# Performance work log

Measured on AMD Instinct MI355X. Metric: run time of the kernel, lower is better.

Reference implementation:

```python
import jax, jax.numpy as jnp
import numpy as np

OUT_FEATURES = 4096
IN_FEATURES = 4096
GROUP_SIZE = 128
NUM_GROUPS = IN_FEATURES // GROUP_SIZE  # 32
PACKED_SIZE = OUT_FEATURES * IN_FEATURES // 8  # 2097152


def setup_inputs() -> dict:
    key = jax.random.key(0)
    k1, k2, k3, k4 = jax.random.split(key, 4)
    x = jax.random.normal(k1, (2, 512, IN_FEATURES), dtype=jnp.float32)
    # random packed 4-bit weights (8 nibbles per int32)
    w_packed = jax.random.randint(k2, (PACKED_SIZE,), jnp.iinfo(jnp.int32).min,
                                  jnp.iinfo(jnp.int32).max, dtype=jnp.int32)
    w_scale = jax.random.uniform(k3, (OUT_FEATURES, NUM_GROUPS), dtype=jnp.float32) * 0.05
    w_zero = jax.random.randint(k4, (OUT_FEATURES, NUM_GROUPS), 0, 8, dtype=jnp.int32)
    return {"x": x, "w_packed": w_packed, "w_scale": w_scale, "w_zero": w_zero}


def _unpack_dequant(w_packed, w_scale, w_zero):
    # Extract 8 nibbles per int32: (v >> (i*4)) & 0xF, i = 0..7
    shifts = jnp.arange(8, dtype=jnp.int32) * 4
    nibbles = (w_packed[:, None] >> shifts[None, :]) & 15  # [packed, 8]
    w4 = nibbles.reshape(-1)  # [out*in], values 0..15
    w4 = jnp.where(w4 >= 8, w4 - 16, w4)  # signed 4-bit -> [-8, 7]
    w_int = w4.reshape(OUT_FEATURES, NUM_GROUPS, GROUP_SIZE).astype(jnp.float32)
    # per-(row, group) dequant: (q - zero) * scale
    w = (w_int - w_zero[:, :, None].astype(jnp.float32)) * w_scale[:, :, None]
    return w.reshape(OUT_FEATURES, IN_FEATURES)


def reference(x, w_packed, w_scale, w_zero):
    weight = _unpack_dequant(w_packed, w_scale, w_zero).astype(x.dtype)
    # F.linear: y = x @ W^T
    return jnp.einsum('bsi,oi->bso', x, weight)
```

## Files before the change

### kernel.cpp

```cpp
#include <hip/hip_runtime.h>
#include <stdint.h>

#define IN_F 4096
#define OUT_F 4096
#define NG 32

typedef __attribute__((ext_vector_type(8))) _Float16 half8;
typedef __attribute__((ext_vector_type(2))) _Float16 half2t;
typedef __attribute__((ext_vector_type(4))) float floatx4;

__global__ __launch_bounds__(256) void prep_kernel(
    const float* __restrict__ x, _Float16* __restrict__ Xh,
    const float* __restrict__ wscale, const int* __restrict__ wzero,
    uint2* __restrict__ SZ, int nxb) {
  int b = blockIdx.x;
  if (b < nxb) {
    int i = b * 256 + threadIdx.x;
    const float4* x4 = (const float4*)x;
    float4 a = x4[2 * i];
    float4 c = x4[2 * i + 1];
    uint4 o;
    o.x = __builtin_bit_cast(unsigned, __builtin_amdgcn_cvt_pkrtz(a.x, c.x));
    o.y = __builtin_bit_cast(unsigned, __builtin_amdgcn_cvt_pkrtz(a.y, c.y));
    o.z = __builtin_bit_cast(unsigned, __builtin_amdgcn_cvt_pkrtz(a.z, c.z));
    o.w = __builtin_bit_cast(unsigned, __builtin_amdgcn_cvt_pkrtz(a.w, c.w));
    ((uint4*)Xh)[i] = o;
  } else {
    int i = (b - nxb) * 256 + threadIdx.x;
    float s = wscale[i];
    int zp = wzero[i];
    _Float16 sh = (_Float16)s;
    _Float16 ch = (_Float16)(float)(1032 + zp);
    unsigned s2 = (unsigned)__builtin_bit_cast(unsigned short, sh) * 0x10001u;
    unsigned c2 = (unsigned)__builtin_bit_cast(unsigned short, ch) * 0x10001u;
    SZ[i] = make_uint2(s2, c2);
  }
}

#define NSTEP 32

__device__ __forceinline__ uint4 dequant8(unsigned v, uint2 szv) {
  unsigned tx = v ^ 0x88888888u;
  half2t s2 = __builtin_bit_cast(half2t, szv.x);
  half2t c2 = __builtin_bit_cast(half2t, szv.y);
  unsigned p0 = (tx & 0x000F000Fu) | 0x64006400u;
  unsigned p1 = ((tx >> 4) & 0x000F000Fu) | 0x64006400u;
  unsigned p2 = ((tx >> 8) & 0x000F000Fu) | 0x64006400u;
  unsigned p3 = ((tx >> 12) & 0x000F000Fu) | 0x64006400u;
  half2t w0 = (__builtin_bit_cast(half2t, p0) - c2) * s2;
  half2t w1 = (__builtin_bit_cast(half2t, p1) - c2) * s2;
  half2t w2 = (__builtin_bit_cast(half2t, p2) - c2) * s2;
  half2t w3 = (__builtin_bit_cast(half2t, p3) - c2) * s2;
  uint4 o;
  o.x = __builtin_bit_cast(unsigned, w0);
  o.y = __builtin_bit_cast(unsigned, w1);
  o.z = __builtin_bit_cast(unsigned, w2);
  o.w = __builtin_bit_cast(unsigned, w3);
  return o;
}

__global__ __launch_bounds__(512, 2) void gemm_fused(
    const _Float16* __restrict__ A, const int* __restrict__ wp,
    const uint2* __restrict__ SZ, float* __restrict__ out,
    int M, int N, int K) {
  __shared__ __align__(16) _Float16 Alds[4 * 8192];
  __shared__ __align__(16) _Float16 Blds[4 * 8192];

  int t = threadIdx.x;
  int wave = t >> 6, lane = t & 63;
  int h = wave >> 2, w2 = wave & 3;
  int wm = (w2 >> 1) * 64, wn = (w2 & 1) * 64;
  int r = lane & 15, quad = lane >> 4, rb = r & 7;
  int bm = blockIdx.y * 128, bn = blockIdx.x * 128;

  floatx4 acc[4][4] = {};

  int kc = t & 7;
  int row0 = t >> 3;
  int row1 = row0 + 64;
  int gkc = kc ^ (row0 & 7);

  const _Float16* Ag = A + (size_t)bm * K;
  const _Float16* gA[4];
  gA[0] = Ag + (size_t)row0 * K + gkc * 8;
  gA[1] = Ag + (size_t)row1 * K + gkc * 8;
  gA[2] = gA[0] + 2048;
  gA[3] = gA[1] + 2048;

  const int* gB[4];
  const uint2* gS[4];
  gB[0] = wp + (size_t)(bn + row0) * (IN_F / 8) + kc;
  gB[1] = wp + (size_t)(bn + row1) * (IN_F / 8) + kc;
  gB[2] = gB[0] + 256;
  gB[3] = gB[1] + 256;
  gS[0] = SZ + (size_t)(bn + row0) * NG;
  gS[1] = SZ + (size_t)(bn + row1) * NG;
  gS[2] = gS[0] + 16;
  gS[3] = gS[1] + 16;

  int bslot = gkc << 3;
  int bofs0 = row0 * 64 + bslot;
  int bofs1 = row1 * 64 + bslot;

  auto STAGE_A = [&](int i, int buf) {
#pragma unroll
    for (int j = 0; j < 4; ++j) {
      const _Float16* src = gA[j] + i * 64;
      int dst = ((j >> 1) * 2 + buf) * 8192 + (t + 512 * (j & 1)) * 8;
      __builtin_amdgcn_global_load_lds(
          (const __attribute__((address_space(1))) void*)src,
          (__attribute__((address_space(3))) void*)(&Alds[dst]), 16, 0, 0);
    }
  };
  auto STAGE_B = [&](const unsigned* v, const uint2* sz, int buf) {
#pragma unroll
    for (int j = 0; j < 4; ++j) {
      int ofs = ((j >> 1) * 2 + buf) * 8192 + ((j & 1) ? bofs1 : bofs0);
      *(uint4*)&Blds[ofs] = dequant8(v[j], sz[j]);
    }
  };
  auto LOADV = [&](int i, unsigned* v, uint2* sz) {
#pragma unroll
    for (int j = 0; j < 4; ++j) {
      v[j] = (unsigned)gB[j][i * 8];
      sz[j] = gS[j][i >> 1];
    }
  };

  unsigned v[4];
  uint2 sz[4];
  LOADV(0, v, sz);
  STAGE_A(0, 0);
  STAGE_B(v, sz, 0);
  LOADV(1, v, sz);
  __syncthreads();

  int cur = 0;
  for (int i = 0; i < NSTEP; ++i) {
    int nxt = cur ^ 1;
    if (i + 1 < NSTEP) {
      STAGE_A(i + 1, nxt);
      STAGE_B(v, sz, nxt);
      int i2 = (i + 2 < NSTEP) ? (i + 2) : (NSTEP - 1);
      LOADV(i2, v, sz);
    }

    const _Float16* Ab = &Alds[(h * 2 + cur) * 8192];
    const _Float16* Bb = &Blds[(h * 2 + cur) * 8192];
#pragma unroll
    for (int ks = 0; ks < 2; ++ks) {
      half8 af[4], bf[4];
#pragma unroll
      for (int mi = 0; mi < 4; ++mi) {
        int R = wm + mi * 16 + r;
        af[mi] = *(const half8*)&Ab[R * 64 + (((ks * 4 + quad) ^ rb) << 3)];
      }
#pragma unroll
      for (int ni = 0; ni < 4; ++ni) {
        int R = wn + ni * 16 + r;
        bf[ni] = *(const half8*)&Bb[R * 64 + (((ks * 4 + quad) ^ rb) << 3)];
      }
#pragma unroll
      for (int mi = 0; mi < 4; ++mi)
#pragma unroll
        for (int ni = 0; ni < 4; ++ni)
          acc[mi][ni] = __builtin_amdgcn_mfma_f32_16x16x32_f16(
              af[mi], bf[ni], acc[mi][ni], 0, 0, 0);
    }
    __syncthreads();
    cur = nxt;
  }

  floatx4* red = (floatx4*)Alds;
  if (h == 1) {
#pragma unroll
    for (int mi = 0; mi < 4; ++mi)
#pragma unroll
      for (int ni = 0; ni < 4; ++ni)
        red[(mi * 4 + ni) * 256 + w2 * 64 + lane] = acc[mi][ni];
  }
  __syncthreads();
  if (h == 0) {
#pragma unroll
    for (int mi = 0; mi < 4; ++mi) {
#pragma unroll
      for (int ni = 0; ni < 4; ++ni) {
        acc[mi][ni] += red[(mi * 4 + ni) * 256 + w2 * 64 + lane];
#pragma unroll
        for (int i = 0; i < 4; ++i) {
          int grow = bm + wm + mi * 16 + quad * 4 + i;
          int gcol = bn + wn + ni * 16 + r;
          out[(size_t)grow * N + gcol] = acc[mi][ni][i];
        }
      }
    }
  }
}

extern "C" void kernel_launch(void* const* d_in, const int* in_sizes, int n_in,
                              void* d_out, int out_size, void* d_ws, size_t ws_size,
                              hipStream_t stream) {
  const float* x = (const float*)d_in[0];
  const int* wp = (const int*)d_in[1];
  const float* wscale = (const float*)d_in[2];
  const int* wzero = (const int*)d_in[3];
  float* out = (float*)d_out;

  int M = in_sizes[0] / IN_F;

  _Float16* Xh = (_Float16*)d_ws;
  uint2* SZ = (uint2*)((char*)d_ws + (size_t)M * IN_F * 2);

  int nxb = (M * IN_F / 8) / 256;
  int nzb = (OUT_F * NG) / 256;
  prep_kernel<<<nxb + nzb, 256, 0, stream>>>(x, Xh, wscale, wzero, SZ, nxb);

  dim3 grid(OUT_F / 128, M / 128);
  gemm_fused<<<grid, 512, 0, stream>>>(Xh, wp, SZ, out, M, OUT_F, IN_F);
}
```

Before: 122.5 us.

## Fuse fp32-to-fp16 activation conversion and scale/zero prep into GEMM kernel

Removes the separate prep kernel. The GEMM now loads fp32 activations into registers, converts them to fp16 and writes them to LDS, and it reads scale and zero directly and packs them per tile. This removes one kernel launch and the global round trip of the fp16 copy of X, at the cost of twice the global bytes for A per tile, because each column tile re-reads fp32 X. It also drops the direct global-to-LDS loads, and it replaces __syncthreads with an lgkmcnt wait plus a barrier. The grid axes are swapped so that blocks sharing a weight tile run adjacently.

```diff
diff --git a/kernel.cpp b/kernel.cpp
--- a/kernel.cpp
+++ b/kernel.cpp
@@ -4,45 +4,20 @@
 #define IN_F 4096
 #define OUT_F 4096
 #define NG 32
+#define NSTEP 32
 
 typedef __attribute__((ext_vector_type(8))) _Float16 half8;
 typedef __attribute__((ext_vector_type(2))) _Float16 half2t;
 typedef __attribute__((ext_vector_type(4))) float floatx4;
 
-__global__ __launch_bounds__(256) void prep_kernel(
-    const float* __restrict__ x, _Float16* __restrict__ Xh,
-    const float* __restrict__ wscale, const int* __restrict__ wzero,
-    uint2* __restrict__ SZ, int nxb) {
-  int b = blockIdx.x;
-  if (b < nxb) {
-    int i = b * 256 + threadIdx.x;
-    const float4* x4 = (const float4*)x;
-    float4 a = x4[2 * i];
-    float4 c = x4[2 * i + 1];
-    uint4 o;
-    o.x = __builtin_bit_cast(unsigned, __builtin_amdgcn_cvt_pkrtz(a.x, c.x));
-    o.y = __builtin_bit_cast(unsigned, __builtin_amdgcn_cvt_pkrtz(a.y, c.y));
-    o.z = __builtin_bit_cast(unsigned, __builtin_amdgcn_cvt_pkrtz(a.z, c.z));
-    o.w = __builtin_bit_cast(unsigned, __builtin_amdgcn_cvt_pkrtz(a.w, c.w));
-    ((uint4*)Xh)[i] = o;
-  } else {
-    int i = (b - nxb) * 256 + threadIdx.x;
-    float s = wscale[i];
-    int zp = wzero[i];
-    _Float16 sh = (_Float16)s;
-    _Float16 ch = (_Float16)(float)(1032 + zp);
-    unsigned s2 = (unsigned)__builtin_bit_cast(unsigned short, sh) * 0x10001u;
-    unsigned c2 = (unsigned)__builtin_bit_cast(unsigned short, ch) * 0x10001u;
-    SZ[i] = make_uint2(s2, c2);
-  }
-}
-
-#define NSTEP 32
-
-__device__ __forceinline__ uint4 dequant8(unsigned v, uint2 szv) {
+__device__ __forceinline__ unsigned pkh(float a, float b) {
+  return __builtin_bit_cast(unsigned, __builtin_amdgcn_cvt_pkrtz(a, b));
+}
+
+__device__ __forceinline__ uint4 dequant8(unsigned v, unsigned s2u, unsigned c2u) {
   unsigned tx = v ^ 0x88888888u;
-  half2t s2 = __builtin_bit_cast(half2t, szv.x);
-  half2t c2 = __builtin_bit_cast(half2t, szv.y);
+  half2t s2 = __builtin_bit_cast(half2t, s2u);
+  half2t c2 = __builtin_bit_cast(half2t, c2u);
   unsigned p0 = (tx & 0x000F000Fu) | 0x64006400u;
   unsigned p1 = ((tx >> 4) & 0x000F000Fu) | 0x64006400u;
   unsigned p2 = ((tx >> 8) & 0x000F000Fu) | 0x64006400u;
@@ -59,90 +34,103 @@
   return o;
 }
 
+__device__ __forceinline__ void sync_lds() {
+  asm volatile("s_waitcnt lgkmcnt(0)" ::: "memory");
+  __builtin_amdgcn_s_barrier();
+}
+
 __global__ __launch_bounds__(512, 2) void gemm_fused(
-    const _Float16* __restrict__ A, const int* __restrict__ wp,
-    const uint2* __restrict__ SZ, float* __restrict__ out,
-    int M, int N, int K) {
+    const float* __restrict__ X, const int* __restrict__ wp,
+    const float* __restrict__ wscale, const int* __restrict__ wzero,
+    float* __restrict__ out, int M, int N, int K) {
   __shared__ __align__(16) _Float16 Alds[4 * 8192];
   __shared__ __align__(16) _Float16 Blds[4 * 8192];
 
-  int t = threadIdx.x;
-  int wave = t >> 6, lane = t & 63;
-  int h = wave >> 2, w2 = wave & 3;
-  int wm = (w2 >> 1) * 64, wn = (w2 & 1) * 64;
-  int r = lane & 15, quad = lane >> 4, rb = r & 7;
-  int bm = blockIdx.y * 128, bn = blockIdx.x * 128;
+  const int t = threadIdx.x;
+  const int wave = t >> 6, lane = t & 63;
+  const int h = wave >> 2, w2 = wave & 3;
+  const int wm = (w2 >> 1) * 64, wn = (w2 & 1) * 64;
+  const int r = lane & 15, quad = lane >> 4, rb = r & 7;
+  const int bm = blockIdx.x * 128, bn = blockIdx.y * 128;
 
   floatx4 acc[4][4] = {};
 
-  int kc = t & 7;
-  int row0 = t >> 3;
-  int row1 = row0 + 64;
-  int gkc = kc ^ (row0 & 7);
-
-  const _Float16* Ag = A + (size_t)bm * K;
-  const _Float16* gA[4];
-  gA[0] = Ag + (size_t)row0 * K + gkc * 8;
-  gA[1] = Ag + (size_t)row1 * K + gkc * 8;
-  gA[2] = gA[0] + 2048;
-  gA[3] = gA[1] + 2048;
-
-  const int* gB[4];
-  const uint2* gS[4];
-  gB[0] = wp + (size_t)(bn + row0) * (IN_F / 8) + kc;
-  gB[1] = wp + (size_t)(bn + row1) * (IN_F / 8) + kc;
-  gB[2] = gB[0] + 256;
-  gB[3] = gB[1] + 256;
-  gS[0] = SZ + (size_t)(bn + row0) * NG;
-  gS[1] = SZ + (size_t)(bn + row1) * NG;
-  gS[2] = gS[0] + 16;
-  gS[3] = gS[1] + 16;
-
-  int bslot = gkc << 3;
-  int bofs0 = row0 * 64 + bslot;
-  int bofs1 = row1 * 64 + bslot;
-
-  auto STAGE_A = [&](int i, int buf) {
+  const int arow = t >> 2, kq = t & 3;
+  const float* gX0 = X + (size_t)(bm + arow) * K + kq * 16;
+  const int aslot0 = arow * 64 + (((kq * 2 + 0) ^ (arow & 7)) << 3);
+  const int aslot1 = arow * 64 + (((kq * 2 + 1) ^ (arow & 7)) << 3);
+
+  const int brow0 = t >> 3, kc8 = t & 7;
+  const int* gB0 = wp + (size_t)(bn + brow0) * (IN_F / 8) + kc8;
+  const int* gB1 = wp + (size_t)(bn + brow0 + 64) * (IN_F / 8) + kc8;
+  const float* gS0 = wscale + (size_t)(bn + brow0) * NG;
+  const float* gS1 = wscale + (size_t)(bn + brow0 + 64) * NG;
+  const int* gZ0 = wzero + (size_t)(bn + brow0) * NG;
+  const int* gZ1 = wzero + (size_t)(bn + brow0 + 64) * NG;
+  const int bslot0 = brow0 * 64 + ((kc8 ^ (brow0 & 7)) << 3);
+  const int bslot1 = (brow0 + 64) * 64 + ((kc8 ^ (brow0 & 7)) << 3);
+
+  float4 ar[2][4];
+  unsigned bv[4];
+  float bs[4];
+  int bz[4];
+
+  auto ISSUE = [&](int i) {
+    const float* p0 = gX0 + i * 64;
+#pragma unroll
+    for (int q = 0; q < 4; ++q) ar[0][q] = ((const float4*)p0)[q];
+    const float* p1 = p0 + 2048;
+#pragma unroll
+    for (int q = 0; q < 4; ++q) ar[1][q] = ((const float4*)p1)[q];
+    bv[0] = (unsigned)gB0[i * 8];
+    bv[1] = (unsigned)gB1[i * 8];
+    bv[2] = (unsigned)gB0[i * 8 + 256];
+    bv[3] = (unsigned)gB1[i * 8 + 256];
+    int g0 = i >> 1;
+    bs[0] = gS0[g0];      bz[0] = gZ0[g0];
+    bs[1] = gS1[g0];      bz[1] = gZ1[g0];
+    bs[2] = gS0[g0 + 16]; bz[2] = gZ0[g0 + 16];
+    bs[3] = gS1[g0 + 16]; bz[3] = gZ1[g0 + 16];
+  };
+
+  auto WRITE = [&](int buf) {
+#pragma unroll
+    for (int hh = 0; hh < 2; ++hh) {
+      uint4 u0, u1;
+      u0.x = pkh(ar[hh][0].x, ar[hh][1].x);
+      u0.y = pkh(ar[hh][0].y, ar[hh][1].y);
+      u0.z = pkh(ar[hh][0].z, ar[hh][1].z);
+      u0.w = pkh(ar[hh][0].w, ar[hh][1].w);
+      u1.x = pkh(ar[hh][2].x, ar[hh][3].x);
+      u1.y = pkh(ar[hh][2].y, ar[hh][3].y);
+      u1.z = pkh(ar[hh][2].z, ar[hh][3].z);
+      u1.w = pkh(ar[hh][2].w, ar[hh][3].w);
+      _Float16* base = &Alds[(hh * 2 + buf) * 8192];
+      *(uint4*)&base[aslot0] = u0;
+      *(uint4*)&base[aslot1] = u1;
+    }
 #pragma unroll
     for (int j = 0; j < 4; ++j) {
-      const _Float16* src = gA[j] + i * 64;
-      int dst = ((j >> 1) * 2 + buf) * 8192 + (t + 512 * (j & 1)) * 8;
-      __builtin_amdgcn_global_load_lds(
-          (const __attribute__((address_space(1))) void*)src,
-          (__attribute__((address_space(3))) void*)(&Alds[dst]), 16, 0, 0);
+      _Float16 sh = (_Float16)bs[j];
+      _Float16 ch = (_Float16)(float)(1032 + bz[j]);
+      unsigned s2 = (unsigned)__builtin_bit_cast(unsigned short, sh) * 0x10001u;
+      unsigned c2 = (unsigned)__builtin_bit_cast(unsigned short, ch) * 0x10001u;
+      int ofs = ((j >> 1) * 2 + buf) * 8192 + ((j & 1) ? bslot1 : bslot0);
+      *(uint4*)&Blds[ofs] = dequant8(bv[j], s2, c2);
     }
   };
-  auto STAGE_B = [&](const unsigned* v, const uint2* sz, int buf) {
-#pragma unroll
-    for (int j = 0; j < 4; ++j) {
-      int ofs = ((j >> 1) * 2 + buf) * 8192 + ((j & 1) ? bofs1 : bofs0);
-      *(uint4*)&Blds[ofs] = dequant8(v[j], sz[j]);
-    }
-  };
-  auto LOADV = [&](int i, unsigned* v, uint2* sz) {
-#pragma unroll
-    for (int j = 0; j < 4; ++j) {
-      v[j] = (unsigned)gB[j][i * 8];
-      sz[j] = gS[j][i >> 1];
-    }
-  };
-
-  unsigned v[4];
-  uint2 sz[4];
-  LOADV(0, v, sz);
-  STAGE_A(0, 0);
-  STAGE_B(v, sz, 0);
-  LOADV(1, v, sz);
-  __syncthreads();
+
+  ISSUE(0);
+  WRITE(0);
+  ISSUE(1);
+  sync_lds();
 
   int cur = 0;
   for (int i = 0; i < NSTEP; ++i) {
-    int nxt = cur ^ 1;
+    const int nxt = cur ^ 1;
     if (i + 1 < NSTEP) {
-      STAGE_A(i + 1, nxt);
-      STAGE_B(v, sz, nxt);
-      int i2 = (i + 2 < NSTEP) ? (i + 2) : (NSTEP - 1);
-      LOADV(i2, v, sz);
+      WRITE(nxt);
+      ISSUE(i + 2 < NSTEP ? i + 2 : NSTEP - 1);
     }
 
     const _Float16* Ab = &Alds[(h * 2 + cur) * 8192];
@@ -167,7 +155,7 @@
           acc[mi][ni] = __builtin_amdgcn_mfma_f32_16x16x32_f16(
               af[mi], bf[ni], acc[mi][ni], 0, 0, 0);
     }
-    __syncthreads();
+    sync_lds();
     cur = nxt;
   }
 
@@ -208,13 +196,6 @@
 
   int M = in_sizes[0] / IN_F;
 
-  _Float16* Xh = (_Float16*)d_ws;
-  uint2* SZ = (uint2*)((char*)d_ws + (size_t)M * IN_F * 2);
-
-  int nxb = (M * IN_F / 8) / 256;
-  int nzb = (OUT_F * NG) / 256;
-  prep_kernel<<<nxb + nzb, 256, 0, stream>>>(x, Xh, wscale, wzero, SZ, nxb);
-
-  dim3 grid(OUT_F / 128, M / 128);
-  gemm_fused<<<grid, 512, 0, stream>>>(Xh, wp, SZ, out, M, OUT_F, IN_F);
-}
+  dim3 grid(M / 128, OUT_F / 128);
+  gemm_fused<<<grid, 512, 0, stream>>>(x, wp, wscale, wzero, out, M, OUT_F, IN_F);
+}
```

Result: slower. 151.0 us (+23.3%).

## Dequantize weights directly into MFMA B-fragments in registers, dropping B LDS staging

Applied to the files above, without the earlier changes.

Each wave now loads packed int4 words straight from global memory in the exact lane layout the MFMA B operand needs, then dequantizes them in registers, so the B shared-memory buffer, its stores and its reads are gone. Scale/zero packing moves from the prep kernel into the GEMM loop, reading the raw float and int arrays with a one-step prefetch. The grid is transposed so blocks sharing a weight tile are adjacent. In exchange, every wave redundantly dequantizes its own B fragments and issues uncoalesced 4-byte global loads, and register pressure rises.

```diff
diff --git a/kernel.cpp b/kernel.cpp
--- a/kernel.cpp
+++ b/kernel.cpp
@@ -4,45 +4,34 @@
 #define IN_F 4096
 #define OUT_F 4096
 #define NG 32
+#define NSTEP 32
 
 typedef __attribute__((ext_vector_type(8))) _Float16 half8;
 typedef __attribute__((ext_vector_type(2))) _Float16 half2t;
 typedef __attribute__((ext_vector_type(4))) float floatx4;
 
+__device__ __forceinline__ unsigned pkh(float a, float b) {
+  return __builtin_bit_cast(unsigned, __builtin_amdgcn_cvt_pkrtz(a, b));
+}
+
 __global__ __launch_bounds__(256) void prep_kernel(
-    const float* __restrict__ x, _Float16* __restrict__ Xh,
-    const float* __restrict__ wscale, const int* __restrict__ wzero,
-    uint2* __restrict__ SZ, int nxb) {
-  int b = blockIdx.x;
-  if (b < nxb) {
-    int i = b * 256 + threadIdx.x;
-    const float4* x4 = (const float4*)x;
-    float4 a = x4[2 * i];
-    float4 c = x4[2 * i + 1];
-    uint4 o;
-    o.x = __builtin_bit_cast(unsigned, __builtin_amdgcn_cvt_pkrtz(a.x, c.x));
-    o.y = __builtin_bit_cast(unsigned, __builtin_amdgcn_cvt_pkrtz(a.y, c.y));
-    o.z = __builtin_bit_cast(unsigned, __builtin_amdgcn_cvt_pkrtz(a.z, c.z));
-    o.w = __builtin_bit_cast(unsigned, __builtin_amdgcn_cvt_pkrtz(a.w, c.w));
-    ((uint4*)Xh)[i] = o;
-  } else {
-    int i = (b - nxb) * 256 + threadIdx.x;
-    float s = wscale[i];
-    int zp = wzero[i];
-    _Float16 sh = (_Float16)s;
-    _Float16 ch = (_Float16)(float)(1032 + zp);
-    unsigned s2 = (unsigned)__builtin_bit_cast(unsigned short, sh) * 0x10001u;
-    unsigned c2 = (unsigned)__builtin_bit_cast(unsigned short, ch) * 0x10001u;
-    SZ[i] = make_uint2(s2, c2);
-  }
-}
-
-#define NSTEP 32
-
-__device__ __forceinline__ uint4 dequant8(unsigned v, uint2 szv) {
+    const float* __restrict__ x, _Float16* __restrict__ Xh) {
+  int i = blockIdx.x * 256 + threadIdx.x;
+  const float4* x4 = (const float4*)x;
+  float4 a = x4[2 * i];
+  float4 c = x4[2 * i + 1];
+  uint4 o;
+  o.x = pkh(a.x, c.x);
+  o.y = pkh(a.y, c.y);
+  o.z = pkh(a.z, c.z);
+  o.w = pkh(a.w, c.w);
+  ((uint4*)Xh)[i] = o;
+}
+
+__device__ __forceinline__ half8 dequant8(unsigned v, unsigned s2u, unsigned c2u) {
   unsigned tx = v ^ 0x88888888u;
-  half2t s2 = __builtin_bit_cast(half2t, szv.x);
-  half2t c2 = __builtin_bit_cast(half2t, szv.y);
+  half2t s2 = __builtin_bit_cast(half2t, s2u);
+  half2t c2 = __builtin_bit_cast(half2t, c2u);
   unsigned p0 = (tx & 0x000F000Fu) | 0x64006400u;
   unsigned p1 = ((tx >> 4) & 0x000F000Fu) | 0x64006400u;
   unsigned p2 = ((tx >> 8) & 0x000F000Fu) | 0x64006400u;
@@ -56,30 +45,26 @@
   o.y = __builtin_bit_cast(unsigned, w1);
   o.z = __builtin_bit_cast(unsigned, w2);
   o.w = __builtin_bit_cast(unsigned, w3);
-  return o;
+  return __builtin_bit_cast(half8, o);
 }
 
 __global__ __launch_bounds__(512, 2) void gemm_fused(
     const _Float16* __restrict__ A, const int* __restrict__ wp,
-    const uint2* __restrict__ SZ, float* __restrict__ out,
-    int M, int N, int K) {
+    const float* __restrict__ wscale, const int* __restrict__ wzero,
+    float* __restrict__ out, int M, int N, int K) {
   __shared__ __align__(16) _Float16 Alds[4 * 8192];
-  __shared__ __align__(16) _Float16 Blds[4 * 8192];
-
-  int t = threadIdx.x;
-  int wave = t >> 6, lane = t & 63;
-  int h = wave >> 2, w2 = wave & 3;
-  int wm = (w2 >> 1) * 64, wn = (w2 & 1) * 64;
-  int r = lane & 15, quad = lane >> 4, rb = r & 7;
-  int bm = blockIdx.y * 128, bn = blockIdx.x * 128;
+
+  const int t = threadIdx.x;
+  const int wave = t >> 6, lane = t & 63;
+  const int h = wave >> 2, w2 = wave & 3;
+  const int wm = (w2 >> 1) * 64, wn = (w2 & 1) * 64;
+  const int r = lane & 15, quad = lane >> 4, rb = r & 7;
+  const int bm = blockIdx.x * 128, bn = blockIdx.y * 128;
 
   floatx4 acc[4][4] = {};
 
-  int kc = t & 7;
-  int row0 = t >> 3;
-  int row1 = row0 + 64;
-  int gkc = kc ^ (row0 & 7);
-
+  const int kc = t & 7, row0 = t >> 3, row1 = row0 + 64;
+  const int gkc = kc ^ (row0 & 7);
   const _Float16* Ag = A + (size_t)bm * K;
   const _Float16* gA[4];
   gA[0] = Ag + (size_t)row0 * K + gkc * 8;
@@ -87,21 +72,6 @@
   gA[2] = gA[0] + 2048;
   gA[3] = gA[1] + 2048;
 
-  const int* gB[4];
-  const uint2* gS[4];
-  gB[0] = wp + (size_t)(bn + row0) * (IN_F / 8) + kc;
-  gB[1] = wp + (size_t)(bn + row1) * (IN_F / 8) + kc;
-  gB[2] = gB[0] + 256;
-  gB[3] = gB[1] + 256;
-  gS[0] = SZ + (size_t)(bn + row0) * NG;
-  gS[1] = SZ + (size_t)(bn + row1) * NG;
-  gS[2] = gS[0] + 16;
-  gS[3] = gS[1] + 16;
-
-  int bslot = gkc << 3;
-  int bofs0 = row0 * 64 + bslot;
-  int bofs1 = row1 * 64 + bslot;
-
   auto STAGE_A = [&](int i, int buf) {
 #pragma unroll
     for (int j = 0; j < 4; ++j) {
@@ -112,41 +82,62 @@
           (__attribute__((address_space(3))) void*)(&Alds[dst]), 16, 0, 0);
     }
   };
-  auto STAGE_B = [&](const unsigned* v, const uint2* sz, int buf) {
-#pragma unroll
-    for (int j = 0; j < 4; ++j) {
-      int ofs = ((j >> 1) * 2 + buf) * 8192 + ((j & 1) ? bofs1 : bofs0);
-      *(uint4*)&Blds[ofs] = dequant8(v[j], sz[j]);
-    }
-  };
-  auto LOADV = [&](int i, unsigned* v, uint2* sz) {
-#pragma unroll
-    for (int j = 0; j < 4; ++j) {
-      v[j] = (unsigned)gB[j][i * 8];
-      sz[j] = gS[j][i >> 1];
-    }
-  };
-
-  unsigned v[4];
-  uint2 sz[4];
-  LOADV(0, v, sz);
+
+  unsigned boff[4];
+  unsigned goff[4];
+#pragma unroll
+  for (int ni = 0; ni < 4; ++ni) {
+    unsigned nrow = (unsigned)(bn + wn + ni * 16 + r);
+    boff[ni] = (nrow * (IN_F / 8) + (unsigned)(h * 256 + quad)) * 4u;
+    goff[ni] = nrow * NG + (unsigned)(h * 16);
+  }
+  const char* wp8 = (const char*)wp;
+
+  unsigned bq[8], bqn[8];
+  unsigned s2[4], c2[4];
+  float sfn[4];
+  int zfn[4];
+
+  auto LOADB = [&](int i, unsigned* dst) {
+#pragma unroll
+    for (int ni = 0; ni < 4; ++ni)
+#pragma unroll
+      for (int ks = 0; ks < 2; ++ks)
+        dst[ni * 2 + ks] =
+            *(const unsigned*)(wp8 + boff[ni] + (unsigned)(i * 32 + ks * 16));
+  };
+  auto LOADS = [&](int i) {
+    int g = i >> 1;
+#pragma unroll
+    for (int ni = 0; ni < 4; ++ni) {
+      sfn[ni] = wscale[goff[ni] + g];
+      zfn[ni] = wzero[goff[ni] + g];
+    }
+  };
+  auto PACKS = [&]() {
+#pragma unroll
+    for (int ni = 0; ni < 4; ++ni) {
+      _Float16 sh = (_Float16)sfn[ni];
+      _Float16 ch = (_Float16)(float)(1032 + zfn[ni]);
+      s2[ni] = (unsigned)__builtin_bit_cast(unsigned short, sh) * 0x10001u;
+      c2[ni] = (unsigned)__builtin_bit_cast(unsigned short, ch) * 0x10001u;
+    }
+  };
+
   STAGE_A(0, 0);
-  STAGE_B(v, sz, 0);
-  LOADV(1, v, sz);
+  LOADB(0, bq);
+  LOADS(0);
+  PACKS();
+  LOADB(1, bqn);
+  LOADS(1);
   __syncthreads();
 
   int cur = 0;
   for (int i = 0; i < NSTEP; ++i) {
-    int nxt = cur ^ 1;
-    if (i + 1 < NSTEP) {
-      STAGE_A(i + 1, nxt);
-      STAGE_B(v, sz, nxt);
-      int i2 = (i + 2 < NSTEP) ? (i + 2) : (NSTEP - 1);
-      LOADV(i2, v, sz);
-    }
+    const int nxt = cur ^ 1;
+    if (i + 1 < NSTEP) STAGE_A(i + 1, nxt);
 
     const _Float16* Ab = &Alds[(h * 2 + cur) * 8192];
-    const _Float16* Bb = &Blds[(h * 2 + cur) * 8192];
 #pragma unroll
     for (int ks = 0; ks < 2; ++ks) {
       half8 af[4], bf[4];
@@ -156,16 +147,24 @@
         af[mi] = *(const half8*)&Ab[R * 64 + (((ks * 4 + quad) ^ rb) << 3)];
       }
 #pragma unroll
-      for (int ni = 0; ni < 4; ++ni) {
-        int R = wn + ni * 16 + r;
-        bf[ni] = *(const half8*)&Bb[R * 64 + (((ks * 4 + quad) ^ rb) << 3)];
-      }
+      for (int ni = 0; ni < 4; ++ni)
+        bf[ni] = dequant8(bq[ni * 2 + ks], s2[ni], c2[ni]);
 #pragma unroll
       for (int mi = 0; mi < 4; ++mi)
 #pragma unroll
         for (int ni = 0; ni < 4; ++ni)
           acc[mi][ni] = __builtin_amdgcn_mfma_f32_16x16x32_f16(
               af[mi], bf[ni], acc[mi][ni], 0, 0, 0);
+    }
+
+    if (i + 1 < NSTEP) {
+#pragma unroll
+      for (int j2 = 0; j2 < 8; ++j2) bq[j2] = bqn[j2];
+      PACKS();
+      if (i + 2 < NSTEP) {
+        LOADB(i + 2, bqn);
+        LOADS(i + 2);
+      }
     }
     __syncthreads();
     cur = nxt;
@@ -209,12 +208,10 @@
   int M = in_sizes[0] / IN_F;
 
   _Float16* Xh = (_Float16*)d_ws;
-  uint2* SZ = (uint2*)((char*)d_ws + (size_t)M * IN_F * 2);
 
   int nxb = (M * IN_F / 8) / 256;
-  int nzb = (OUT_F * NG) / 256;
-  prep_kernel<<<nxb + nzb, 256, 0, stream>>>(x, Xh, wscale, wzero, SZ, nxb);
-
-  dim3 grid(OUT_F / 128, M / 128);
-  gemm_fused<<<grid, 512, 0, stream>>>(Xh, wp, SZ, out, M, OUT_F, IN_F);
-}
+  prep_kernel<<<nxb, 256, 0, stream>>>(x, Xh);
+
+  dim3 grid(M / 128, OUT_F / 128);
+  gemm_fused<<<grid, 512, 0, stream>>>(Xh, wp, wscale, wzero, out, M, OUT_F, IN_F);
+}
```

Measured after the change: 210.1 us. 71.5% more time.

## Triple-buffer A tiles in LDS with manual waitcnt and barrier scheduling

Applied to the files above, without the earlier changes.

The A-operand LDS staging goes from double to triple buffering, so global_load_lds for step i+2 is issued while step i computes. The generic __syncthreads is replaced by explicit s_waitcnt vmcnt(4)/lgkmcnt(0), s_barrier and sched_barrier, which lets the in-flight loads for the next tile stay outstanding across the barrier. The loop is unrolled by two, alternating register sets for the packed weight prefetch. This raises LDS use per block, which may limit two blocks per CU, and depends on the hand-picked vmcnt values being right.

```diff
diff --git a/kernel.cpp b/kernel.cpp
--- a/kernel.cpp
+++ b/kernel.cpp
@@ -4,10 +4,15 @@
 #define IN_F 4096
 #define OUT_F 4096
 #define NG 32
+#define NSTEP 32
 
 typedef __attribute__((ext_vector_type(8))) _Float16 half8;
 typedef __attribute__((ext_vector_type(2))) _Float16 half2t;
 typedef __attribute__((ext_vector_type(4))) float floatx4;
+
+__device__ __forceinline__ unsigned pkh(float a, float b) {
+  return __builtin_bit_cast(unsigned, __builtin_amdgcn_cvt_pkrtz(a, b));
+}
 
 __global__ __launch_bounds__(256) void prep_kernel(
     const float* __restrict__ x, _Float16* __restrict__ Xh,
@@ -20,10 +25,10 @@
     float4 a = x4[2 * i];
     float4 c = x4[2 * i + 1];
     uint4 o;
-    o.x = __builtin_bit_cast(unsigned, __builtin_amdgcn_cvt_pkrtz(a.x, c.x));
-    o.y = __builtin_bit_cast(unsigned, __builtin_amdgcn_cvt_pkrtz(a.y, c.y));
-    o.z = __builtin_bit_cast(unsigned, __builtin_amdgcn_cvt_pkrtz(a.z, c.z));
-    o.w = __builtin_bit_cast(unsigned, __builtin_amdgcn_cvt_pkrtz(a.w, c.w));
+    o.x = pkh(a.x, c.x);
+    o.y = pkh(a.y, c.y);
+    o.z = pkh(a.z, c.z);
+    o.w = pkh(a.w, c.w);
     ((uint4*)Xh)[i] = o;
   } else {
     int i = (b - nxb) * 256 + threadIdx.x;
@@ -36,8 +41,6 @@
     SZ[i] = make_uint2(s2, c2);
   }
 }
-
-#define NSTEP 32
 
 __device__ __forceinline__ uint4 dequant8(unsigned v, uint2 szv) {
   unsigned tx = v ^ 0x88888888u;
@@ -63,23 +66,20 @@
     const _Float16* __restrict__ A, const int* __restrict__ wp,
     const uint2* __restrict__ SZ, float* __restrict__ out,
     int M, int N, int K) {
-  __shared__ __align__(16) _Float16 Alds[4 * 8192];
+  __shared__ __align__(16) _Float16 Alds[6 * 8192];
   __shared__ __align__(16) _Float16 Blds[4 * 8192];
 
-  int t = threadIdx.x;
-  int wave = t >> 6, lane = t & 63;
-  int h = wave >> 2, w2 = wave & 3;
-  int wm = (w2 >> 1) * 64, wn = (w2 & 1) * 64;
-  int r = lane & 15, quad = lane >> 4, rb = r & 7;
-  int bm = blockIdx.y * 128, bn = blockIdx.x * 128;
+  const int t = threadIdx.x;
+  const int wave = t >> 6, lane = t & 63;
+  const int h = wave >> 2, w2 = wave & 3;
+  const int wm = (w2 >> 1) * 64, wn = (w2 & 1) * 64;
+  const int r = lane & 15, quad = lane >> 4, rb = r & 7;
+  const int bm = blockIdx.y * 128, bn = blockIdx.x * 128;
 
   floatx4 acc[4][4] = {};
 
-  int kc = t & 7;
-  int row0 = t >> 3;
-  int row1 = row0 + 64;
-  int gkc = kc ^ (row0 & 7);
-
+  const int kc = t & 7, row0 = t >> 3, row1 = row0 + 64;
+  const int gkc = kc ^ (row0 & 7);
   const _Float16* Ag = A + (size_t)bm * K;
   const _Float16* gA[4];
   gA[0] = Ag + (size_t)row0 * K + gkc * 8;
@@ -87,88 +87,96 @@
   gA[2] = gA[0] + 2048;
   gA[3] = gA[1] + 2048;
 
-  const int* gB[4];
-  const uint2* gS[4];
-  gB[0] = wp + (size_t)(bn + row0) * (IN_F / 8) + kc;
-  gB[1] = wp + (size_t)(bn + row1) * (IN_F / 8) + kc;
-  gB[2] = gB[0] + 256;
-  gB[3] = gB[1] + 256;
-  gS[0] = SZ + (size_t)(bn + row0) * NG;
-  gS[1] = SZ + (size_t)(bn + row1) * NG;
-  gS[2] = gS[0] + 16;
-  gS[3] = gS[1] + 16;
-
-  int bslot = gkc << 3;
-  int bofs0 = row0 * 64 + bslot;
-  int bofs1 = row1 * 64 + bslot;
-
-  auto STAGE_A = [&](int i, int buf) {
-#pragma unroll
-    for (int j = 0; j < 4; ++j) {
-      const _Float16* src = gA[j] + i * 64;
-      int dst = ((j >> 1) * 2 + buf) * 8192 + (t + 512 * (j & 1)) * 8;
-      __builtin_amdgcn_global_load_lds(
-          (const __attribute__((address_space(1))) void*)src,
-          (__attribute__((address_space(3))) void*)(&Alds[dst]), 16, 0, 0);
-    }
-  };
-  auto STAGE_B = [&](const unsigned* v, const uint2* sz, int buf) {
-#pragma unroll
-    for (int j = 0; j < 4; ++j) {
-      int ofs = ((j >> 1) * 2 + buf) * 8192 + ((j & 1) ? bofs1 : bofs0);
-      *(uint4*)&Blds[ofs] = dequant8(v[j], sz[j]);
-    }
-  };
-  auto LOADV = [&](int i, unsigned* v, uint2* sz) {
-#pragma unroll
-    for (int j = 0; j < 4; ++j) {
-      v[j] = (unsigned)gB[j][i * 8];
-      sz[j] = gS[j][i >> 1];
-    }
-  };
-
-  unsigned v[4];
-  uint2 sz[4];
-  LOADV(0, v, sz);
+#define STAGE_A(i, st)                                                        \
+  {                                                                           \
+    _Pragma("unroll") for (int j = 0; j < 4; ++j) {                           \
+      const _Float16* src = gA[j] + (i) * 64;                                 \
+      int dst = ((st) * 2 + (j >> 1)) * 8192 + (t + 512 * (j & 1)) * 8;       \
+      __builtin_amdgcn_global_load_lds(                                       \
+          (const __attribute__((address_space(1))) void*)src,                 \
+          (__attribute__((address_space(3))) void*)(&Alds[dst]), 16, 0, 0);   \
+    }                                                                         \
+  }
+
+  const int brow0 = t >> 3, kc8 = t & 7;
+  const int* gB0 = wp + (size_t)(bn + brow0) * (IN_F / 8) + kc8;
+  const int* gB1 = wp + (size_t)(bn + brow0 + 64) * (IN_F / 8) + kc8;
+  const uint2* gS0 = SZ + (size_t)(bn + brow0) * NG;
+  const uint2* gS1 = SZ + (size_t)(bn + brow0 + 64) * NG;
+  const int bslot0 = brow0 * 64 + ((kc8 ^ (brow0 & 7)) << 3);
+  const int bslot1 = (brow0 + 64) * 64 + ((kc8 ^ (brow0 & 7)) << 3);
+
+#define LOADV(i, v, s)                                                        \
+  {                                                                           \
+    v[0] = (unsigned)gB0[(i) * 8];                                            \
+    v[1] = (unsigned)gB1[(i) * 8];                                            \
+    v[2] = (unsigned)gB0[(i) * 8 + 256];                                      \
+    v[3] = (unsigned)gB1[(i) * 8 + 256];                                      \
+    int g0 = (i) >> 1;                                                        \
+    s[0] = gS0[g0];                                                           \
+    s[1] = gS1[g0];                                                           \
+    s[2] = gS0[g0 + 16];                                                      \
+    s[3] = gS1[g0 + 16];                                                      \
+  }
+
+#define WRITE_B(v, s, dstbuf)                                                 \
+  {                                                                           \
+    _Pragma("unroll") for (int j = 0; j < 4; ++j) {                           \
+      int ofs = ((dstbuf) * 2 + (j >> 1)) * 8192 + ((j & 1) ? bslot1 : bslot0); \
+      *(uint4*)&Blds[ofs] = dequant8(v[j], s[j]);                             \
+    }                                                                         \
+  }
+
+  unsigned vA[4], vB[4];
+  uint2 sA[4], sB[4];
+  int ra = 0, rw = 2;
+
+  LOADV(0, vB, sB);
+  WRITE_B(vB, sB, 0);
+  LOADV(1, vA, sA);
+  asm volatile("" ::: "memory");
   STAGE_A(0, 0);
-  STAGE_B(v, sz, 0);
-  LOADV(1, v, sz);
-  __syncthreads();
-
-  int cur = 0;
-  for (int i = 0; i < NSTEP; ++i) {
-    int nxt = cur ^ 1;
-    if (i + 1 < NSTEP) {
-      STAGE_A(i + 1, nxt);
-      STAGE_B(v, sz, nxt);
-      int i2 = (i + 2 < NSTEP) ? (i + 2) : (NSTEP - 1);
-      LOADV(i2, v, sz);
-    }
-
-    const _Float16* Ab = &Alds[(h * 2 + cur) * 8192];
-    const _Float16* Bb = &Blds[(h * 2 + cur) * 8192];
-#pragma unroll
-    for (int ks = 0; ks < 2; ++ks) {
-      half8 af[4], bf[4];
-#pragma unroll
-      for (int mi = 0; mi < 4; ++mi) {
-        int R = wm + mi * 16 + r;
-        af[mi] = *(const half8*)&Ab[R * 64 + (((ks * 4 + quad) ^ rb) << 3)];
-      }
-#pragma unroll
-      for (int ni = 0; ni < 4; ++ni) {
-        int R = wn + ni * 16 + r;
-        bf[ni] = *(const half8*)&Bb[R * 64 + (((ks * 4 + quad) ^ rb) << 3)];
-      }
-#pragma unroll
-      for (int mi = 0; mi < 4; ++mi)
-#pragma unroll
-        for (int ni = 0; ni < 4; ++ni)
-          acc[mi][ni] = __builtin_amdgcn_mfma_f32_16x16x32_f16(
-              af[mi], bf[ni], acc[mi][ni], 0, 0, 0);
-    }
-    __syncthreads();
-    cur = nxt;
+  STAGE_A(1, 1);
+  asm volatile("s_waitcnt vmcnt(4) lgkmcnt(0)" ::: "memory");
+  __builtin_amdgcn_s_barrier();
+  __builtin_amdgcn_sched_barrier(0);
+
+#define STEP(i, p, vC, sC, vL, sL)                                            \
+  {                                                                           \
+    if ((i) + 1 < NSTEP) WRITE_B(vC, sC, (p) ^ 1);                            \
+    if ((i) + 2 < NSTEP) LOADV((i) + 2, vL, sL);                              \
+    asm volatile("" ::: "memory");         \
+    if ((i) + 2 < NSTEP) STAGE_A((i) + 2, rw);                                \
+    const _Float16* Ab = &Alds[(ra * 2 + h) * 8192];                          \
+    const _Float16* Bb = &Blds[((p) * 2 + h) * 8192];                         \
+    _Pragma("unroll") for (int ks = 0; ks < 2; ++ks) {                        \
+      half8 af[4], bf[4];                                                     \
+      _Pragma("unroll") for (int mi = 0; mi < 4; ++mi) {                      \
+        int R = wm + mi * 16 + r;                                             \
+        af[mi] = *(const half8*)&Ab[R * 64 + (((ks * 4 + quad) ^ rb) << 3)];  \
+      }                                                                       \
+      _Pragma("unroll") for (int ni = 0; ni < 4; ++ni) {                      \
+        int R = wn + ni * 16 + r;                                             \
+        bf[ni] = *(const half8*)&Bb[R * 64 + (((ks * 4 + quad) ^ rb) << 3)];  \
+      }                                                                       \
+      _Pragma("unroll") for (int mi = 0; mi < 4; ++mi)                        \
+        _Pragma("unroll") for (int ni = 0; ni < 4; ++ni)                      \
+          acc[mi][ni] = __builtin_amdgcn_mfma_f32_16x16x32_f16(               \
+              af[mi], bf[ni], acc[mi][ni], 0, 0, 0);                          \
+    }                                                                         \
+    if ((i) + 2 < NSTEP)                                                      \
+      asm volatile("s_waitcnt vmcnt(4) lgkmcnt(0)" ::: "memory");             \
+    else                                                                      \
+      asm volatile("s_waitcnt vmcnt(0) lgkmcnt(0)" ::: "memory");             \
+    __builtin_amdgcn_s_barrier();                                             \
+    __builtin_amdgcn_sched_barrier(0);                                        \
+    ra = (ra + 1 == 3) ? 0 : ra + 1;                                          \
+    rw = (rw + 1 == 3) ? 0 : rw + 1;                                          \
+  }
+
+  for (int i = 0; i < NSTEP; i += 2) {
+    STEP(i, 0, vA, sA, vB, sB);
+    STEP(i + 1, 1, vB, sB, vA, sA);
   }
 
   floatx4* red = (floatx4*)Alds;
```

Measured after the change: 128.1 us. +4.6%, slower.
